# Kernel tuning notes

Hardware: AMD Instinct MI355X
Metric: run time of the kernel (lower is better)

Reference implementation:

```python
import jax, jax.numpy as jnp
import numpy as np

EPS = 1e-9
ALPHA = 1.0
BETA = 6.0
TOPK = 13
NUM_CLASSES = 80


def _make_boxes(key, shape, img=640.0, wh_min=8.0, wh_max=128.0):
    k1, k2 = jax.random.split(key)
    cxy = jax.random.uniform(k1, shape[:-1] + (2,)) * img
    wh = wh_min + jax.random.uniform(k2, shape[:-1] + (2,)) * (wh_max - wh_min)
    return jnp.concatenate([cxy - wh / 2, cxy + wh / 2], axis=-1)


def setup_inputs() -> dict:
    key = jax.random.key(0)
    ks = jax.random.split(key, 5)
    B, N, C, M = 16, 8400, NUM_CLASSES, 64
    pd_scores = jax.random.normal(ks[0], (B, N, C), dtype=jnp.float32)  # logits
    pd_bboxes = _make_boxes(ks[1], (B, N, 4))
    anc_points = jax.random.uniform(ks[2], (N, 2)) * 640.0
    gt_labels = jax.random.randint(ks[3], (B, M, 1), 0, C).astype(jnp.int64)
    gt_bboxes = _make_boxes(ks[4], (B, M, 4), wh_min=16.0, wh_max=256.0)
    mask_gt = jnp.ones((B, M, 1), dtype=jnp.float32)
    return {"pd_scores": pd_scores, "pd_bboxes": pd_bboxes, "anc_points": anc_points,
            "gt_labels": gt_labels, "gt_bboxes": gt_bboxes, "mask_gt": mask_gt}


def _pairwise_iou(gt_bboxes, pd_bboxes):
    # gt: (B,M,4), pd: (B,N,4) -> (B,M,N)
    a1 = gt_bboxes[:, :, None, :2]
    a2 = gt_bboxes[:, :, None, 2:]
    b1 = pd_bboxes[:, None, :, :2]
    b2 = pd_bboxes[:, None, :, 2:]
    inter = jnp.clip(jnp.minimum(a2, b2) - jnp.maximum(a1, b1), 0.0).prod(-1)
    area_a = (a2 - a1).prod(-1)
    area_b = (b2 - b1).prod(-1)
    return inter / jnp.maximum(area_a + area_b - inter, EPS)


def _tal_assign(pd_scores, pd_bboxes, anc_points, gt_labels, gt_bboxes, mask_gt):
    B, N, C = pd_scores.shape
    M = gt_labels.shape[1]
    ps = jax.nn.sigmoid(pd_scores)  # input_is_logits=True
    mask_gt_bool = mask_gt[..., 0] > 0.5  # (B,M)

    # centers-in-boxes mask (B,M,N)
    xy = anc_points[None, None, :, :]
    lt = gt_bboxes[:, :, None, :2]
    rb = gt_bboxes[:, :, None, 2:]
    deltas = jnp.concatenate([xy - lt, rb - xy], axis=-1)  # (B,M,N,4)
    mask_in_gts = deltas.min(-1) > EPS
    valid = mask_in_gts & mask_gt_bool[:, :, None]

    # alignment metric: score(gt class)^alpha * IoU^beta, zero outside valid
    gt_ids = jnp.clip(gt_labels[..., 0], 0)  # (B,M)
    scores_t = jnp.swapaxes(ps, 1, 2)  # (B,C,N)
    bbox_scores = jnp.take_along_axis(scores_t, gt_ids[:, :, None], axis=1)  # (B,M,N)
    ious = _pairwise_iou(gt_bboxes, pd_bboxes)
    ious = jnp.where(valid, ious, 0.0)
    align = jnp.where(valid, (bbox_scores ** ALPHA) * (ious ** BETA), 0.0)

    # top-k anchors per GT along anchor dim
    topv, topi = jax.lax.top_k(align, TOPK)  # (B,M,K)
    sel = (topv > EPS) & mask_gt_bool[:, :, None]
    bi = jnp.arange(B)[:, None, None]
    mi = jnp.arange(M)[None, :, None]
    cnt = jnp.zeros((B, M, N), jnp.int32).at[bi, mi, topi].add(sel.astype(jnp.int32))
    topk_mask = cnt > 0
    mask_pos = (topk_mask & valid).astype(jnp.float32)  # (B,M,N)

    # resolve anchors assigned to multiple GTs: keep highest IoU GT
    fg = mask_pos.sum(axis=1)  # (B,N)
    multi = (fg > 1)[:, None, :]  # (B,1,N)
    best_gt = jnp.argmax(ious, axis=1)  # (B,N)
    is_max = jnp.swapaxes(jax.nn.one_hot(best_gt, M, dtype=mask_pos.dtype), 1, 2)  # (B,M,N)
    mask_pos = jnp.where(multi, is_max, mask_pos)
    fg_mask = mask_pos.sum(axis=1)  # (B,N)
    tgt_gt_idx = jnp.argmax(mask_pos, axis=1)  # (B,N)

    # gather targets
    target_labels = jnp.take_along_axis(gt_labels[..., 0], tgt_gt_idx, axis=1)  # (B,N)
    target_bboxes = jnp.take_along_axis(gt_bboxes, tgt_gt_idx[..., None], axis=1)  # (B,N,4)

    # normalized classification targets
    align = align * mask_pos
    max_align = align.max(axis=1, keepdims=True) + EPS  # (B,1,N)
    per_anchor = (align / max_align * (ious * mask_pos)).sum(axis=1)  # (B,N)
    onehot = jax.nn.one_hot(target_labels, C, dtype=jnp.float32)
    cls_targets = onehot * per_anchor[..., None]  # (B,N,C)
    return target_labels, target_bboxes, cls_targets, fg_mask > 0, tgt_gt_idx


def reference(pd_scores, pd_bboxes, anc_points, gt_labels, gt_bboxes, mask_gt):
    return _tal_assign(pd_scores, pd_bboxes, anc_points, gt_labels, gt_bboxes, mask_gt)
```

## Files before the change

kernel.cpp:

```cpp
#include <hip/hip_runtime.h>
#include <math.h>

#define BB 16
#define NN 8400
#define CC 80
#define MM 64
#define KTOP 13
#define FEPS 1e-9f
#define CAP 2048
#define RPW 8

typedef float floatx4 __attribute__((ext_vector_type(4)));
typedef unsigned long long u64;

#define OFF_O1 134400
#define OFF_O2 672000
#define OFF_O3 11424000
#define OFF_O4 11558400

#define ZERO_N (1024 + 3 * 134400)

__device__ __forceinline__ float iou_pair(const float4 g, const float4 p) {
    float ix1 = fmaxf(g.x, p.x);
    float iy1 = fmaxf(g.y, p.y);
    float ix2 = fminf(g.z, p.z);
    float iy2 = fminf(g.w, p.w);
    float iw = fmaxf(ix2 - ix1, 0.0f);
    float ih = fmaxf(iy2 - iy1, 0.0f);
    float inter = iw * ih;
    float aa = (g.z - g.x) * (g.w - g.y);
    float ab = (p.z - p.x) * (p.w - p.y);
    float uni = fmaxf(aa + ab - inter, FEPS);
    return inter / uni;
}

__global__ __launch_bounds__(256) void k_zero(int* __restrict__ p)
{
    int i = blockIdx.x * 256 + threadIdx.x;
    if (i < ZERO_N) p[i] = 0;
}

__global__ __launch_bounds__(256) void k_align_emit(
    const float* __restrict__ pd_scores, const float* __restrict__ pd_bboxes,
    const float* __restrict__ anc, const int* __restrict__ gt_labels,
    const float* __restrict__ gt_bboxes, const float* __restrict__ mask_gt,
    int* __restrict__ ccnt, u64* __restrict__ cand)
{
    const int b = blockIdx.y;
    const int tid = threadIdx.x;
    const int n0 = blockIdx.x * 256;
    const int n = n0 + tid;

    __shared__ float4 gtb[MM];
    __shared__ int    labS[MM];
    __shared__ int    hcnt[MM];
    __shared__ int    gbase[MM];
    __shared__ u64    maskS[256];
    __shared__ float4 srows4[640];
    __shared__ float4 pbbS[32];

    if (tid < MM) {
        float4 g = *(const float4*)&gt_bboxes[(size_t)(b * MM + tid) * 4];
        if (mask_gt[b * MM + tid] <= 0.5f)
            g = make_float4(1e30f, 1e30f, -1e30f, -1e30f);
        gtb[tid] = g;
        int lb = gt_labels[b * MM + tid];
        labS[tid] = lb > 0 ? lb : 0;
        hcnt[tid] = 0;
    }
    __syncthreads();

    float ax = 0.0f, ay = 0.0f;
    const bool inb = n < NN;
    if (inb) { float2 a2 = *(const float2*)&anc[2 * n]; ax = a2.x; ay = a2.y; }

    u64 mask = 0ull;
    #pragma unroll 8
    for (int m = 0; m < MM; ++m) {
        float4 g = gtb[m];
        float d1 = ax - g.x, d2 = ay - g.y, d3 = g.z - ax, d4 = g.w - ay;
        if (inb && fminf(fminf(d1, d2), fminf(d3, d4)) > FEPS)
            mask |= 1ull << m;
    }
    maskS[tid] = mask;

    u64 t = mask;
    while (t) { int m = __ffsll(t) - 1; t &= t - 1; atomicAdd(&hcnt[m], 1); }
    __syncthreads();
    if (tid < MM && hcnt[tid] > 0) {
        gbase[tid] = atomicAdd(&ccnt[b * MM + tid], hcnt[tid]);
        hcnt[tid] = 0;
    }

    const float4* src4 = (const float4*)(pd_scores + (size_t)b * NN * CC);
    for (int sub = 0; sub < 8; ++sub) {
        const int la0 = sub * 32;
        const int gn0 = n0 + la0;
        __syncthreads();
        {
            const int base4 = gn0 * 20;
            #pragma unroll
            for (int k = tid; k < 640; k += 256) {
                int gf = base4 + k;
                srows4[k] = (gf < NN * 20) ? src4[gf]
                                           : make_float4(0.f, 0.f, 0.f, 0.f);
            }
            if (tid < 32) {
                int gn = gn0 + tid;
                pbbS[tid] = (gn < NN)
                    ? *(const float4*)&pd_bboxes[((size_t)b * NN + gn) * 4]
                    : make_float4(0.f, 0.f, 0.f, 0.f);
            }
        }
        __syncthreads();

        const int la = la0 + (tid >> 3);
        const int r = tid & 7;
        u64 tt = maskS[la] & (0x0101010101010101ull << r);
        if (tt) {
            const float4 p = pbbS[la - la0];
            const float* row = (const float*)srows4 + (la - la0) * 80;
            const int gn = n0 + la;
            while (tt) {
                int m = __ffsll(tt) - 1; tt &= tt - 1;
                float io = iou_pair(gtb[m], p);
                float x = row[labS[m]];
                float s = 1.0f / (1.0f + expf(-x));
                float i2 = io * io;
                unsigned key = __float_as_uint(s * (i2 * i2 * i2));
                int slot = gbase[m] + atomicAdd(&hcnt[m], 1);
                if (slot < CAP)
                    cand[(size_t)(b * MM + m) * CAP + slot] =
                        ((u64)key << 32) | (unsigned)(NN - gn);
            }
        }
    }
}

__global__ __launch_bounds__(256) void k_topk(
    const int* __restrict__ ccnt, const u64* __restrict__ cand,
    int* __restrict__ cntb, int* __restrict__ mselb, float* __restrict__ aselb)
{
    const int bm = blockIdx.x;
    const int b = bm >> 6, m = bm & 63;
    const int tid = threadIdx.x;
    const int lane = tid & 63;
    const int wid = tid >> 6;

    __shared__ u64 cmerge[64];

    const unsigned epskey = __float_as_uint(FEPS);
    const int count = min(ccnt[bm], CAP);
    const u64* list = cand + (size_t)bm * CAP;

    u64 e[RPW];
    #pragma unroll
    for (int j = 0; j < RPW; ++j) {
        int i = tid + j * 256;
        e[j] = (i < count) ? list[i] : 0ull;
    }

    {
        u64 lm = 0ull;
        #pragma unroll
        for (int j = 0; j < RPW; ++j) if (e[j] > lm) lm = e[j];

        u64 winv = 0ull;
        for (int r = 0; r < KTOP; ++r) {
            u64 bv = lm;
            #pragma unroll
            for (int off = 32; off > 0; off >>= 1) {
                u64 ov = __shfl_xor(bv, off, 64);
                if (ov > bv) bv = ov;
            }
            if ((unsigned)(bv >> 32) <= epskey) break;
            if (lane == r) winv = bv;
            if (lm == bv) {
                #pragma unroll
                for (int j = 0; j < RPW; ++j) if (e[j] == bv) e[j] = 0ull;
                lm = 0ull;
                #pragma unroll
                for (int j = 0; j < RPW; ++j) if (e[j] > lm) lm = e[j];
            }
        }
        if (lane < KTOP) cmerge[wid * KTOP + lane] = winv;
        if (wid == 0 && lane >= 4 * KTOP) cmerge[lane] = 0ull;
    }
    __syncthreads();

    if (wid == 0) {
        u64 v = cmerge[lane];
        u64 winv = 0ull;
        for (int r = 0; r < KTOP; ++r) {
            u64 bv = v;
            #pragma unroll
            for (int off = 32; off > 0; off >>= 1) {
                u64 ov = __shfl_xor(bv, off, 64);
                if (ov > bv) bv = ov;
            }
            if ((unsigned)(bv >> 32) <= epskey) break;
            if (lane == r) winv = bv;
            if (v == bv) v = 0ull;
        }
        if (lane < KTOP) {
            unsigned hk = (unsigned)(winv >> 32);
            if (hk > epskey) {
                int n = NN - (int)(winv & 0xFFFFFFFFull);
                int ai = b * NN + n;
                atomicAdd(&cntb[ai], 1);
                atomicAdd(&mselb[ai], m);
                atomicAdd(&aselb[ai], __uint_as_float(hk));
            }
        }
    }
}

__global__ __launch_bounds__(256) void k_assign_cls(
    const float* __restrict__ pd_scores, const float* __restrict__ pd_bboxes,
    const float* __restrict__ anc, const int* __restrict__ gt_labels,
    const float* __restrict__ gt_bboxes, const float* __restrict__ mask_gt,
    const int* __restrict__ cntb, const int* __restrict__ mselb,
    const float* __restrict__ aselb,
    float* __restrict__ out0, float* __restrict__ out1,
    float* __restrict__ out3, float* __restrict__ out4,
    floatx4* __restrict__ cls4)
{
    const int b = blockIdx.y;
    const int n0 = blockIdx.x * 256;
    const int tid = threadIdx.x;
    const int n = n0 + tid;

    __shared__ float4 gtb[MM];
    __shared__ int    labS[MM];
    __shared__ float  mgS[MM];
    __shared__ int    labL[256];
    __shared__ float  perL[256];

    if (tid < MM) {
        int m = tid;
        gtb[m]  = *(const float4*)&gt_bboxes[(size_t)(b * MM + m) * 4];
        labS[m] = gt_labels[b * MM + m];
        mgS[m]  = mask_gt[b * MM + m];
    }
    __syncthreads();

    float per = 0.0f, fg = 0.0f;
    int mstar = 0;

    if (n < NN) {
        const size_t idx = (size_t)b * NN + n;
        const int cnt = cntb[idx];
        if (cnt > 0) {
            fg = 1.0f;
            const float4 p = *(const float4*)&pd_bboxes[idx * 4];
            if (cnt == 1) {
                mstar = mselb[idx];
                float a = aselb[idx];
                float io = iou_pair(gtb[mstar], p);
                per = a / (a + FEPS) * io;
            } else {
                float2 a2 = *(const float2*)&anc[2 * n];
                float bestI = -1.0f; int bestM = 0;
                for (int m = 0; m < MM; ++m) {
                    float4 gg = gtb[m];
                    float d1 = a2.x - gg.x, d2 = a2.y - gg.y;
                    float d3 = gg.z - a2.x, d4 = gg.w - a2.y;
                    bool valid = (fminf(fminf(d1, d2), fminf(d3, d4)) > FEPS) &&
                                 (mgS[m] > 0.5f);
                    float io = valid ? iou_pair(gg, p) : 0.0f;
                    if (io > bestI) { bestI = io; bestM = m; }
                }
                mstar = bestM;
                float io = bestI;
                int lb = labS[mstar]; int lbc = lb > 0 ? lb : 0;
                float x = pd_scores[idx * CC + lbc];
                float s = 1.0f / (1.0f + expf(-x));
                float i2 = io * io;
                float a = s * (i2 * i2 * i2);
                per = a / (a + FEPS) * io;
            }
        }
        out0[idx] = (float)labS[mstar];
        ((float4*)out1)[idx] = gtb[mstar];
        out3[idx] = fg;
        out4[idx] = (float)mstar;
    }
    labL[tid] = (n < NN) ? labS[mstar] : 0;
    perL[tid] = per;
    __syncthreads();

    const size_t base4 = ((size_t)b * NN + n0) * 20;
    for (int k = tid; k < 5120; k += 256) {
        int lrow = k / 20;
        int gn = n0 + lrow;
        if (gn >= NN) break;
        int c4 = (k - lrow * 20) * 4;
        int lab = labL[lrow];
        float pr = perL[lrow];
        int d = lab - c4;
        floatx4 v;
        v.x = (d == 0) ? pr : 0.0f;
        v.y = (d == 1) ? pr : 0.0f;
        v.z = (d == 2) ? pr : 0.0f;
        v.w = (d == 3) ? pr : 0.0f;
        __builtin_nontemporal_store(v, &cls4[base4 + k]);
    }
}

extern "C" void kernel_launch(void* const* d_in, const int* in_sizes, int n_in,
                              void* d_out, int out_size, void* d_ws, size_t ws_size,
                              hipStream_t stream) {
    const float* pd_scores = (const float*)d_in[0];
    const float* pd_bboxes = (const float*)d_in[1];
    const float* anc       = (const float*)d_in[2];
    const int*   gt_labels = (const int*)d_in[3];
    const float* gt_bboxes = (const float*)d_in[4];
    const float* mask_gt   = (const float*)d_in[5];

    float* out  = (float*)d_out;
    float* out0 = out;
    float* out1 = out + OFF_O1;
    float* out2 = out + OFF_O2;
    float* out3 = out + OFF_O3;
    float* out4 = out + OFF_O4;

    int*   ws_i  = (int*)d_ws;
    int*   ccnt  = ws_i;
    int*   cntb  = ws_i + 1024;
    int*   mselb = ws_i + 1024 + 134400;
    float* aselb = (float*)(ws_i + 1024 + 2 * 134400);
    u64*   cand  = (u64*)((char*)d_ws + (size_t)ZERO_N * 4);

    k_zero<<<dim3((ZERO_N + 255) / 256), dim3(256), 0, stream>>>(ws_i);

    k_align_emit<<<dim3((NN + 255) / 256, BB), dim3(256), 0, stream>>>(
        pd_scores, pd_bboxes, anc, gt_labels, gt_bboxes, mask_gt, ccnt, cand);

    k_topk<<<dim3(BB * MM), dim3(256), 0, stream>>>(
        ccnt, cand, cntb, mselb, aselb);

    k_assign_cls<<<dim3((NN + 255) / 256, BB), dim3(256), 0, stream>>>(
        pd_scores, pd_bboxes, anc, gt_labels, gt_bboxes, mask_gt,
        cntb, mselb, aselb, out0, out1, out3, out4, (floatx4*)out2);
}
```

Measured before the change: 71.05 us.

## Restructure align_emit to 64 anchors per block with early score prefetch

The align/emit kernel now handles 64 anchors per block instead of 256. Four threads share each anchor and each tests 16 GTs, replacing the per-thread 64-bit mask. The score rows for all 64 anchors are loaded into registers at kernel start, so the global loads overlap the mask computation, and the 8-step load/sync loop is gone. This gives about four times as many blocks and fewer barriers, at the cost of more shared memory per block and more atomics on the shared histograms.

```diff
diff --git a/kernel.cpp b/kernel.cpp
--- a/kernel.cpp
+++ b/kernel.cpp
@@ -47,17 +47,27 @@
     int* __restrict__ ccnt, u64* __restrict__ cand)
 {
     const int b = blockIdx.y;
+    const int n0 = blockIdx.x * 64;
     const int tid = threadIdx.x;
-    const int n0 = blockIdx.x * 256;
-    const int n = n0 + tid;
-
+    const int a = tid >> 2;
+    const int q = tid & 3;
+
+    __shared__ float4 srows4[1280];
     __shared__ float4 gtb[MM];
+    __shared__ float4 pbbS[64];
+    __shared__ float2 ancS[64];
     __shared__ int    labS[MM];
-    __shared__ int    hcnt[MM];
-    __shared__ int    gbase[MM];
-    __shared__ u64    maskS[256];
-    __shared__ float4 srows4[640];
-    __shared__ float4 pbbS[32];
+    __shared__ unsigned short maskS16[256];
+    __shared__ int hcnt[MM], hslot[MM], gbase[MM];
+
+    const float4* src4 = (const float4*)(pd_scores + (size_t)b * NN * CC);
+    const int base4 = n0 * 20;
+    const int lim = NN * 20 - base4;
+    float4 r0 = (tid        < lim) ? src4[base4 + tid       ] : make_float4(0,0,0,0);
+    float4 r1 = (tid + 256  < lim) ? src4[base4 + tid + 256 ] : make_float4(0,0,0,0);
+    float4 r2 = (tid + 512  < lim) ? src4[base4 + tid + 512 ] : make_float4(0,0,0,0);
+    float4 r3 = (tid + 768  < lim) ? src4[base4 + tid + 768 ] : make_float4(0,0,0,0);
+    float4 r4 = (tid + 1024 < lim) ? src4[base4 + tid + 1024] : make_float4(0,0,0,0);
 
     if (tid < MM) {
         float4 g = *(const float4*)&gt_bboxes[(size_t)(b * MM + tid) * 4];
@@ -67,68 +77,64 @@
         int lb = gt_labels[b * MM + tid];
         labS[tid] = lb > 0 ? lb : 0;
         hcnt[tid] = 0;
-    }
-    __syncthreads();
-
-    float ax = 0.0f, ay = 0.0f;
-    const bool inb = n < NN;
-    if (inb) { float2 a2 = *(const float2*)&anc[2 * n]; ax = a2.x; ay = a2.y; }
-
-    u64 mask = 0ull;
-    #pragma unroll 8
-    for (int m = 0; m < MM; ++m) {
-        float4 g = gtb[m];
-        float d1 = ax - g.x, d2 = ay - g.y, d3 = g.z - ax, d4 = g.w - ay;
-        if (inb && fminf(fminf(d1, d2), fminf(d3, d4)) > FEPS)
-            mask |= 1ull << m;
-    }
-    maskS[tid] = mask;
-
-    u64 t = mask;
-    while (t) { int m = __ffsll(t) - 1; t &= t - 1; atomicAdd(&hcnt[m], 1); }
-    __syncthreads();
-    if (tid < MM && hcnt[tid] > 0) {
+        hslot[tid] = 0;
+    }
+    if (tid < 64) {
+        int gn = n0 + tid;
+        pbbS[tid] = (gn < NN)
+            ? *(const float4*)&pd_bboxes[((size_t)b * NN + gn) * 4]
+            : make_float4(0.f, 0.f, 0.f, 0.f);
+        ancS[tid] = (gn < NN) ? *(const float2*)&anc[2 * gn]
+                              : make_float2(0.f, 0.f);
+    }
+    __syncthreads();
+
+    {
+        unsigned short pm = 0;
+        if (n0 + a < NN) {
+            float ax = ancS[a].x, ay = ancS[a].y;
+            #pragma unroll
+            for (int mm = 0; mm < 16; ++mm) {
+                float4 g = gtb[q * 16 + mm];
+                float d1 = ax - g.x, d2 = ay - g.y;
+                float d3 = g.z - ax, d4 = g.w - ay;
+                if (fminf(fminf(d1, d2), fminf(d3, d4)) > FEPS)
+                    pm |= (unsigned short)(1u << mm);
+            }
+        }
+        maskS16[tid] = pm;
+        unsigned t16 = pm;
+        while (t16) {
+            int mm = __ffs(t16) - 1; t16 &= t16 - 1;
+            atomicAdd(&hcnt[q * 16 + mm], 1);
+        }
+    }
+    srows4[tid       ] = r0;
+    srows4[tid + 256 ] = r1;
+    srows4[tid + 512 ] = r2;
+    srows4[tid + 768 ] = r3;
+    srows4[tid + 1024] = r4;
+    __syncthreads();
+
+    if (tid < MM && hcnt[tid] > 0)
         gbase[tid] = atomicAdd(&ccnt[b * MM + tid], hcnt[tid]);
-        hcnt[tid] = 0;
-    }
-
-    const float4* src4 = (const float4*)(pd_scores + (size_t)b * NN * CC);
-    for (int sub = 0; sub < 8; ++sub) {
-        const int la0 = sub * 32;
-        const int gn0 = n0 + la0;
-        __syncthreads();
-        {
-            const int base4 = gn0 * 20;
-            #pragma unroll
-            for (int k = tid; k < 640; k += 256) {
-                int gf = base4 + k;
-                srows4[k] = (gf < NN * 20) ? src4[gf]
-                                           : make_float4(0.f, 0.f, 0.f, 0.f);
-            }
-            if (tid < 32) {
-                int gn = gn0 + tid;
-                pbbS[tid] = (gn < NN)
-                    ? *(const float4*)&pd_bboxes[((size_t)b * NN + gn) * 4]
-                    : make_float4(0.f, 0.f, 0.f, 0.f);
-            }
-        }
-        __syncthreads();
-
-        const int la = la0 + (tid >> 3);
-        const int r = tid & 7;
-        u64 tt = maskS[la] & (0x0101010101010101ull << r);
-        if (tt) {
-            const float4 p = pbbS[la - la0];
-            const float* row = (const float*)srows4 + (la - la0) * 80;
-            const int gn = n0 + la;
-            while (tt) {
-                int m = __ffsll(tt) - 1; tt &= tt - 1;
+    __syncthreads();
+
+    {
+        unsigned t16 = maskS16[tid];
+        if (t16) {
+            const float4 p = pbbS[a];
+            const float* row = (const float*)srows4 + a * 80;
+            const int gn = n0 + a;
+            while (t16) {
+                int mm = __ffs(t16) - 1; t16 &= t16 - 1;
+                int m = q * 16 + mm;
                 float io = iou_pair(gtb[m], p);
                 float x = row[labS[m]];
                 float s = 1.0f / (1.0f + expf(-x));
                 float i2 = io * io;
                 unsigned key = __float_as_uint(s * (i2 * i2 * i2));
-                int slot = gbase[m] + atomicAdd(&hcnt[m], 1);
+                int slot = gbase[m] + atomicAdd(&hslot[m], 1);
                 if (slot < CAP)
                     cand[(size_t)(b * MM + m) * CAP + slot] =
                         ((u64)key << 32) | (unsigned)(NN - gn);
@@ -333,7 +339,7 @@
 
     k_zero<<<dim3((ZERO_N + 255) / 256), dim3(256), 0, stream>>>(ws_i);
 
-    k_align_emit<<<dim3((NN + 255) / 256, BB), dim3(256), 0, stream>>>(
+    k_align_emit<<<dim3((NN + 63) / 64, BB), dim3(256), 0, stream>>>(
         pd_scores, pd_bboxes, anc, gt_labels, gt_bboxes, mask_gt, ccnt, cand);
 
     k_topk<<<dim3(BB * MM), dim3(256), 0, stream>>>(
```

New measurement: 61.79 us. 13.0% less time.
